# Performance work log

Measured on AMD Instinct MI355X. Metric: run time of the kernel, lower is better.

Reference implementation:

```python
import jax, jax.numpy as jnp
import numpy as np

N_NODES = 50000
N_EDGES = 800000
IN_SIZE = 128
NUM_HEADS = 8
HEAD_DIM = IN_SIZE // NUM_HEADS  # qk/val head dim = 16


def setup_inputs() -> dict:
    key = jax.random.key(0)
    ks = jax.random.split(key, 16)
    d = IN_SIZE
    lim = 1.0 / np.sqrt(d)
    inp = {
        "in_feats": jax.random.normal(ks[0], (N_NODES, d), jnp.float32),
        "struc_feats": jax.random.normal(ks[1], (N_NODES, d), jnp.float32),
        "edge_weights": jax.random.uniform(ks[2], (N_EDGES,), jnp.float32),
        "ln_scale": jnp.ones((d,), jnp.float32),
        "ln_bias": jnp.zeros((d,), jnp.float32),
        "Ws": jax.random.uniform(ks[3], (d, d), jnp.float32, -lim, lim),
        "bs": jnp.zeros((d,), jnp.float32),
        "Wq": jax.random.uniform(ks[4], (d, d), jnp.float32, -lim, lim),
        "bq": jnp.zeros((d,), jnp.float32),
        "Wk": jax.random.uniform(ks[5], (d, d), jnp.float32, -lim, lim),
        "bk": jnp.zeros((d,), jnp.float32),
        "Wv": jax.random.uniform(ks[6], (d, d), jnp.float32, -lim, lim),
        "bv": jnp.zeros((d,), jnp.float32),
        "Wo": jax.random.uniform(ks[7], (d, d), jnp.float32, -lim, lim),
        "edge_ids": jax.random.randint(ks[8], (2, N_EDGES), 0, N_NODES, jnp.int64)
        if jax.config.jax_enable_x64 else jax.random.randint(ks[8], (2, N_EDGES), 0, N_NODES, jnp.int32),
    }
    return inp


def _layer_norm(x, scale, bias, eps=1e-5):
    mu = jnp.mean(x, axis=-1, keepdims=True)
    var = jnp.var(x, axis=-1, keepdims=True)
    return (x - mu) * jax.lax.rsqrt(var + eps) * scale + bias


def reference(in_feats, struc_feats, edge_weights, ln_scale, ln_bias,
              Ws, bs, Wq, bq, Wk, bk, Wv, bv, Wo, edge_ids):
    N = in_feats.shape[0]
    H, hd = NUM_HEADS, HEAD_DIM

    delta = _layer_norm(in_feats, ln_scale, ln_bias)           # pre-norm
    delta = jax.nn.gelu(delta, approximate=False)               # pre-activation (exact GELU, torch default)
    delta_struc = delta + struc_feats @ Ws.T + bs               # struc_proj add

    qry = (delta_struc @ Wq.T + bq) / np.sqrt(hd)                # [N, qk]
    keyf = delta_struc @ Wk.T + bk                               # [N, qk]
    val = delta @ Wv.T + bv                                      # [N, val]

    src, dst = edge_ids[0], edge_ids[1]                          # out[src] += A[src,dst] * val[dst]
    qe = qry[src].reshape(-1, H, hd)                             # [E, H, hd]
    ke = keyf[dst].reshape(-1, H, hd)                            # [E, H, hd]
    attn = jax.nn.sigmoid(jnp.sum(qe * ke, axis=-1))             # [E, H]
    attn = edge_weights[:, None] * attn

    msgs = attn[:, :, None] * val[dst].reshape(-1, H, hd)        # [E, H, hd]
    agg = jax.ops.segment_sum(msgs.reshape(-1, H * hd), src, num_segments=N)  # [N, val]

    out = agg @ Wo.T                                             # out_proj (no bias)
    return in_feats + out                                        # skip connection
```

## Files before the change

kernel.cpp:

```cpp
#include <hip/hip_runtime.h>
#include <math.h>

#define NF 128

typedef __attribute__((ext_vector_type(8))) short short8;
typedef __attribute__((ext_vector_type(4))) float floatx4;

__device__ __forceinline__ unsigned short f2bf(float f) {
    union { float x; unsigned int i; } c; c.x = f;
    unsigned int r = c.i + 0x7fffu + ((c.i >> 16) & 1u);
    return (unsigned short)(r >> 16);
}
__device__ __forceinline__ float bf2f(unsigned short u) {
    union { unsigned int i; float x; } c; c.i = ((unsigned int)u) << 16;
    return c.x;
}
__device__ __forceinline__ void unpack8(uint4 u, float* f) {
    union { unsigned int i; float x; } c;
    c.i = u.x << 16;          f[0] = c.x;
    c.i = u.x & 0xffff0000u;  f[1] = c.x;
    c.i = u.y << 16;          f[2] = c.x;
    c.i = u.y & 0xffff0000u;  f[3] = c.x;
    c.i = u.z << 16;          f[4] = c.x;
    c.i = u.z & 0xffff0000u;  f[5] = c.x;
    c.i = u.w << 16;          f[6] = c.x;
    c.i = u.w & 0xffff0000u;  f[7] = c.x;
}
__device__ __forceinline__ ushort4 pack4(float a, float b, float c, float d) {
    ushort4 h; h.x = f2bf(a); h.y = f2bf(b); h.z = f2bf(c); h.w = f2bf(d);
    return h;
}

__global__ __launch_bounds__(256) void wconv5_kernel(
    const float* __restrict__ a, const float* __restrict__ b,
    const float* __restrict__ c, const float* __restrict__ d,
    const float* __restrict__ e, unsigned short* __restrict__ o)
{
    int i = blockIdx.x * 256 + threadIdx.x;
    int w = i >> 14, j = i & 16383;
    const float* p = (w == 0) ? a : (w == 1) ? b : (w == 2) ? c : (w == 3) ? d : e;
    o[i] = f2bf(p[j]);
}

__global__ __launch_bounds__(256) void node_a_kernel(
    const float* __restrict__ in_feats, const float* __restrict__ struc,
    const float* __restrict__ gamma, const float* __restrict__ beta,
    const unsigned short* __restrict__ Wsb, const float* __restrict__ bs,
    unsigned short* __restrict__ deltab, unsigned short* __restrict__ dstrb,
    int M, int nt)
{
    __shared__ unsigned short Wl[128][136];
    __shared__ unsigned short Xs2[64][136];

    int tid = threadIdx.x;
    int lane = tid & 63, w = tid >> 6, lg = lane & 15, quad = lane >> 4;
    int lrow = tid >> 2, t4 = tid & 3;

    {
        const uint4* g = (const uint4*)Wsb;
        #pragma unroll
        for (int p = 0; p < 8; ++p) {
            int idx = tid + p * 256;
            *(uint4*)&Wl[idx >> 4][(idx & 15) * 8] = g[idx];
        }
    }
    float bsr[8];
    #pragma unroll
    for (int t = 0; t < 8; ++t) bsr[t] = bs[t * 16 + lg];
    __syncthreads();

    for (int tile = blockIdx.x; tile < nt; tile += gridDim.x) {
        int m0 = tile * 64;
        int gm = m0 + lrow;
        bool vr = gm < M;
        size_t rbase = (size_t)(vr ? gm : 0) * NF;

        uint dreg[16];
        {
            const float4* ip = (const float4*)(in_feats + rbase) + t4 * 8;
            float4 xf[8];
            #pragma unroll
            for (int p = 0; p < 8; ++p) xf[p] = ip[p];
            float s = 0.f, sq = 0.f;
            #pragma unroll
            for (int p = 0; p < 8; ++p) {
                s  += xf[p].x + xf[p].y + xf[p].z + xf[p].w;
                sq += xf[p].x * xf[p].x + xf[p].y * xf[p].y
                    + xf[p].z * xf[p].z + xf[p].w * xf[p].w;
            }
            s  += __shfl_xor(s, 1, 64);  s  += __shfl_xor(s, 2, 64);
            sq += __shfl_xor(sq, 1, 64); sq += __shfl_xor(sq, 2, 64);
            float mu = s * (1.0f / 128.0f);
            float var = sq * (1.0f / 128.0f) - mu * mu;
            float rstd = rsqrtf(var + 1e-5f);
            const float4* gp = (const float4*)gamma + t4 * 8;
            const float4* bp = (const float4*)beta + t4 * 8;
            #pragma unroll
            for (int p = 0; p < 8; ++p) {
                float4 g4 = gp[p], b4 = bp[p];
                float o0 = (xf[p].x - mu) * rstd * g4.x + b4.x;
                float o1 = (xf[p].y - mu) * rstd * g4.y + b4.y;
                float o2 = (xf[p].z - mu) * rstd * g4.z + b4.z;
                float o3 = (xf[p].w - mu) * rstd * g4.w + b4.w;
                o0 = 0.5f * o0 * (1.0f + erff(o0 * 0.70710678118654752f));
                o1 = 0.5f * o1 * (1.0f + erff(o1 * 0.70710678118654752f));
                o2 = 0.5f * o2 * (1.0f + erff(o2 * 0.70710678118654752f));
                o3 = 0.5f * o3 * (1.0f + erff(o3 * 0.70710678118654752f));
                ushort4 h = pack4(o0, o1, o2, o3);
                dreg[p * 2]     = (uint)h.x | ((uint)h.y << 16);
                dreg[p * 2 + 1] = (uint)h.z | ((uint)h.w << 16);
            }
            if (vr) {
                uint4* od = (uint4*)(deltab + (size_t)gm * NF + t4 * 32);
                #pragma unroll
                for (int q = 0; q < 4; ++q)
                    od[q] = make_uint4(dreg[q*4], dreg[q*4+1], dreg[q*4+2], dreg[q*4+3]);
            }
            const float4* sp = (const float4*)(struc + rbase) + t4 * 8;
            #pragma unroll
            for (int p = 0; p < 8; ++p) {
                float4 f = sp[p];
                *(ushort4*)&Xs2[lrow][t4 * 32 + p * 4] = pack4(f.x, f.y, f.z, f.w);
            }
        }

        floatx4 acc[8];
        #pragma unroll
        for (int t = 0; t < 8; ++t) acc[t] = (floatx4){0.f, 0.f, 0.f, 0.f};
        #pragma unroll
        for (int ks = 0; ks < 4; ++ks) {
            short8 a = *(const short8*)&Xs2[w * 16 + lg][ks * 32 + quad * 8];
            #pragma unroll
            for (int t = 0; t < 8; ++t) {
                short8 b = *(const short8*)&Wl[t * 16 + lg][ks * 32 + quad * 8];
                acc[t] = __builtin_amdgcn_mfma_f32_16x16x32_bf16(a, b, acc[t], 0, 0, 0);
            }
        }

        #pragma unroll
        for (int q = 0; q < 4; ++q)
            *(uint4*)&Xs2[lrow][t4 * 32 + q * 8] =
                make_uint4(dreg[q*4], dreg[q*4+1], dreg[q*4+2], dreg[q*4+3]);

        #pragma unroll
        for (int t = 0; t < 8; ++t) {
            int col = t * 16 + lg;
            #pragma unroll
            for (int r = 0; r < 4; ++r) {
                int rl = w * 16 + quad * 4 + r;
                Xs2[rl][col] = f2bf(acc[t][r] + bsr[t] + bf2f(Xs2[rl][col]));
            }
        }
        #pragma unroll
        for (int p = 0; p < 4; ++p) {
            int idx = lane + p * 64;
            int row = w * 16 + (idx >> 4), c16 = idx & 15;
            int gmo = m0 + row;
            if (gmo < M)
                *(uint4*)(dstrb + (size_t)gmo * NF + c16 * 8) = *(const uint4*)&Xs2[row][c16 * 8];
        }
    }
}

__global__ __launch_bounds__(256) void node_qkv_kernel(
    const unsigned short* __restrict__ deltab, const unsigned short* __restrict__ dstrb,
    const unsigned short* __restrict__ Wall, const float* __restrict__ bq,
    const float* __restrict__ bk, const float* __restrict__ bv,
    unsigned short* __restrict__ qb, unsigned short* __restrict__ kvb,
    int M, int nt)
{
    __shared__ unsigned short Wl[128][136];
    __shared__ unsigned short Cst[64][136];

    int tid = threadIdx.x;
    int y = blockIdx.y;
    int lane = tid & 63, w = tid >> 6, lg = lane & 15, quad = lane >> 4;

    const unsigned short* Xg = (y == 2) ? deltab : dstrb;
    const unsigned short* Wg = Wall + (y + 1) * 16384;
    const float* bias = (y == 0) ? bq : (y == 1) ? bk : bv;
    float scale = (y == 0) ? 0.25f : 1.0f;
    unsigned short* outg = (y == 0) ? qb : (y == 1) ? kvb : (kvb + NF);
    int ostride = (y == 0) ? NF : 2 * NF;

    {
        const uint4* g = (const uint4*)Wg;
        #pragma unroll
        for (int p = 0; p < 8; ++p) {
            int idx = tid + p * 256;
            *(uint4*)&Wl[idx >> 4][(idx & 15) * 8] = g[idx];
        }
    }
    float br[8];
    #pragma unroll
    for (int t = 0; t < 8; ++t) br[t] = bias[t * 16 + lg] * scale;
    __syncthreads();

    for (int tile = blockIdx.x; tile < nt; tile += gridDim.x) {
        int m0 = tile * 64;
        int am = m0 + w * 16 + lg;
        const unsigned short* arow = Xg + (size_t)(am < M ? am : 0) * NF + quad * 8;

        floatx4 acc[8];
        #pragma unroll
        for (int t = 0; t < 8; ++t) acc[t] = (floatx4){0.f, 0.f, 0.f, 0.f};
        short8 af[4];
        #pragma unroll
        for (int ks = 0; ks < 4; ++ks) af[ks] = *(const short8*)(arow + ks * 32);
        #pragma unroll
        for (int ks = 0; ks < 4; ++ks) {
            #pragma unroll
            for (int t = 0; t < 8; ++t) {
                short8 b = *(const short8*)&Wl[t * 16 + lg][ks * 32 + quad * 8];
                acc[t] = __builtin_amdgcn_mfma_f32_16x16x32_bf16(af[ks], b, acc[t], 0, 0, 0);
            }
        }
        #pragma unroll
        for (int t = 0; t < 8; ++t) {
            int col = t * 16 + lg;
            #pragma unroll
            for (int r = 0; r < 4; ++r)
                Cst[w * 16 + quad * 4 + r][col] = f2bf(acc[t][r] * scale + br[t]);
        }
        #pragma unroll
        for (int p = 0; p < 4; ++p) {
            int idx = lane + p * 64;
            int row = w * 16 + (idx >> 4), c16 = idx & 15;
            int gm = m0 + row;
            if (gm < M)
                *(uint4*)(outg + (size_t)gm * ostride + c16 * 8) = *(const uint4*)&Cst[row][c16 * 8];
        }
    }
}

__global__ __launch_bounds__(256) void gemm_out_kernel(
    const unsigned short* __restrict__ Xb, const unsigned short* __restrict__ Wb,
    const float* __restrict__ addf, float* __restrict__ Y, int M, int nt)
{
    __shared__ unsigned short Wl[128][136];
    int tid = threadIdx.x;
    int lane = tid & 63, w = tid >> 6, lg = lane & 15, quad = lane >> 4;

    {
        const uint4* g = (const uint4*)Wb;
        #pragma unroll
        for (int p = 0; p < 8; ++p) {
            int idx = tid + p * 256;
            *(uint4*)&Wl[idx >> 4][(idx & 15) * 8] = g[idx];
        }
    }
    __syncthreads();

    for (int tile = blockIdx.x; tile < nt; tile += gridDim.x) {
        int m0 = tile * 64;
        int am = m0 + w * 16 + lg;
        const unsigned short* arow = Xb + (size_t)(am < M ? am : 0) * NF + quad * 8;

        floatx4 acc[8];
        #pragma unroll
        for (int t = 0; t < 8; ++t) acc[t] = (floatx4){0.f, 0.f, 0.f, 0.f};
        short8 af[4];
        #pragma unroll
        for (int ks = 0; ks < 4; ++ks) af[ks] = *(const short8*)(arow + ks * 32);
        #pragma unroll
        for (int ks = 0; ks < 4; ++ks) {
            #pragma unroll
            for (int t = 0; t < 8; ++t) {
                short8 b = *(const short8*)&Wl[t * 16 + lg][ks * 32 + quad * 8];
                acc[t] = __builtin_amdgcn_mfma_f32_16x16x32_bf16(af[ks], b, acc[t], 0, 0, 0);
            }
        }
        #pragma unroll
        for (int t = 0; t < 8; ++t) {
            int col = t * 16 + lg;
            #pragma unroll
            for (int r = 0; r < 4; ++r) {
                int gm = m0 + w * 16 + quad * 4 + r;
                if (gm >= M) continue;
                size_t off = (size_t)gm * NF + col;
                Y[off] = acc[t][r] + addf[off];
            }
        }
    }
}

__global__ void hist_kernel(const int* __restrict__ eid, int* __restrict__ cnt, int E)
{
    int i = blockIdx.x * blockDim.x + threadIdx.x;
    if (i < E) atomicAdd(&cnt[eid[i]], 1);
}

__global__ __launch_bounds__(256) void scan1_kernel(
    const int* __restrict__ cnt, int* __restrict__ bsum, int n)
{
    int base = blockIdx.x * 1024;
    int s = 0;
    #pragma unroll
    for (int p = 0; p < 4; ++p) {
        int i = base + (int)threadIdx.x + p * 256;
        if (i < n) s += cnt[i];
    }
    #pragma unroll
    for (int m = 1; m <= 32; m <<= 1) s += __shfl_xor(s, m, 64);
    __shared__ int ws_[4];
    int wid = threadIdx.x >> 6;
    if ((threadIdx.x & 63) == 0) ws_[wid] = s;
    __syncthreads();
    if (threadIdx.x == 0) bsum[blockIdx.x] = ws_[0] + ws_[1] + ws_[2] + ws_[3];
}

__global__ __launch_bounds__(256) void scan3_kernel(
    const int* __restrict__ cnt, const int* __restrict__ bsum,
    int* __restrict__ row_start, int* __restrict__ cursor, int n, int nb)
{
    __shared__ int base_off;
    int tid = threadIdx.x, lane = tid & 63, wid = tid >> 6;
    if (tid == 0) {
        int a = 0;
        for (int j = 0; j < (int)blockIdx.x; ++j) a += bsum[j];
        base_off = a;
        if ((int)blockIdx.x == nb - 1) {
            int tot = a;
            for (int j = blockIdx.x; j < nb; ++j) tot += bsum[j];
            row_start[n] = tot;
        }
    }
    int base = blockIdx.x * 1024;
    int v[4]; int s = 0;
    #pragma unroll
    for (int p = 0; p < 4; ++p) {
        int i = base + tid * 4 + p;
        v[p] = (i < n) ? cnt[i] : 0;
        s += v[p];
    }
    int ss = s;
    #pragma unroll
    for (int off = 1; off < 64; off <<= 1) {
        int t = __shfl_up(ss, off, 64);
        if (lane >= off) ss += t;
    }
    __shared__ int wsum[4];
    if (lane == 63) wsum[wid] = ss;
    __syncthreads();
    int woff = 0;
    for (int j = 0; j < wid; ++j) woff += wsum[j];
    int a = base_off + woff + (ss - s);
    #pragma unroll
    for (int p = 0; p < 4; ++p) {
        int i = base + tid * 4 + p;
        if (i < n) { row_start[i] = a; cursor[i] = a; a += v[p]; }
    }
}

__global__ void scatter_kernel(const int* __restrict__ eid, const float* __restrict__ ew,
                               int* __restrict__ cursor, int2* __restrict__ edata, int E)
{
    int i = blockIdx.x * blockDim.x + threadIdx.x;
    if (i < E) {
        int src = eid[i];
        int dst = eid[E + i];
        int pos = atomicAdd(&cursor[src], 1);
        edata[pos] = make_int2(dst, __float_as_int(ew[i]));
    }
}

__global__ __launch_bounds__(256) void aggregate_kernel(
    const unsigned short* __restrict__ Q, const unsigned short* __restrict__ kvb,
    const int* __restrict__ row_start, const int2* __restrict__ edata,
    unsigned short* __restrict__ agg, int N)
{
    int node = blockIdx.x * 4 + (threadIdx.x >> 6);
    if (node >= N) return;
    int lane = threadIdx.x & 63;
    int sg = lane >> 4, lg = lane & 15;
    int rs = row_start[node], re = row_start[node + 1];

    float qv[8];
    unpack8(*(const uint4*)(Q + (size_t)node * NF + lg * 8), qv);
    float acc[8];
    #pragma unroll
    for (int j = 0; j < 8; ++j) acc[j] = 0.f;

    int e1 = rs + sg, e2 = rs + sg + 4;
    int2 ed1 = (e1 < re) ? edata[e1] : make_int2(0, 0);
    int2 ed2 = (e2 < re) ? edata[e2] : make_int2(0, 0);

    for (int e0 = rs; e0 < re; e0 += 8) {
        int2 c1 = ed1, c2 = ed2;
        int en1 = e0 + 8 + sg, en2 = en1 + 4;
        ed1 = (en1 < re) ? edata[en1] : make_int2(0, 0);
        ed2 = (en2 < re) ? edata[en2] : make_int2(0, 0);

        const uint4* p1 = (const uint4*)kvb + (size_t)c1.x * 32 + lg;
        const uint4* p2 = (const uint4*)kvb + (size_t)c2.x * 32 + lg;
        uint4 k1u = p1[0], v1u = p1[16];
        uint4 k2u = p2[0], v2u = p2[16];

        float kv1[8], kv2[8];
        unpack8(k1u, kv1);
        unpack8(k2u, kv2);
        float s1 = qv[0] * kv1[0], s2 = qv[0] * kv2[0];
        #pragma unroll
        for (int j = 1; j < 8; ++j) {
            s1 = fmaf(qv[j], kv1[j], s1);
            s2 = fmaf(qv[j], kv2[j], s2);
        }
        s1 += __shfl_xor(s1, 1, 64);
        s2 += __shfl_xor(s2, 1, 64);
        float a1 = __int_as_float(c1.y) / (1.f + __expf(-s1));
        float a2 = __int_as_float(c2.y) / (1.f + __expf(-s2));

        float vv1[8], vv2[8];
        unpack8(v1u, vv1);
        unpack8(v2u, vv2);
        #pragma unroll
        for (int j = 0; j < 8; ++j) {
            acc[j] = fmaf(a1, vv1[j], acc[j]);
            acc[j] = fmaf(a2, vv2[j], acc[j]);
        }
    }
    #pragma unroll
    for (int j = 0; j < 8; ++j) {
        acc[j] += __shfl_xor(acc[j], 16, 64);
        acc[j] += __shfl_xor(acc[j], 32, 64);
    }
    if (sg == 0) {
        unsigned short* o = agg + (size_t)node * NF + lg * 8;
        *(ushort4*)o       = pack4(acc[0], acc[1], acc[2], acc[3]);
        *(ushort4*)(o + 4) = pack4(acc[4], acc[5], acc[6], acc[7]);
    }
}

extern "C" void kernel_launch(void* const* d_in, const int* in_sizes, int n_in,
                              void* d_out, int out_size, void* d_ws, size_t ws_size,
                              hipStream_t stream)
{
    const float* in_feats = (const float*)d_in[0];
    const float* struc    = (const float*)d_in[1];
    const float* eweights = (const float*)d_in[2];
    const float* ln_scale = (const float*)d_in[3];
    const float* ln_bias  = (const float*)d_in[4];
    const float* Ws       = (const float*)d_in[5];
    const float* bs       = (const float*)d_in[6];
    const float* Wq       = (const float*)d_in[7];
    const float* bq       = (const float*)d_in[8];
    const float* Wk       = (const float*)d_in[9];
    const float* bk       = (const float*)d_in[10];
    const float* Wv       = (const float*)d_in[11];
    const float* bv       = (const float*)d_in[12];
    const float* Wo       = (const float*)d_in[13];
    const int*   edge_ids = (const int*)d_in[14];
    float* out = (float*)d_out;

    int N = in_sizes[0] / NF;
    int E = in_sizes[2];

    size_t F = (size_t)N * NF;
    unsigned short* deltab = (unsigned short*)d_ws;
    unsigned short* dstrb  = deltab + F;
    unsigned short* qb     = dstrb + F;
    unsigned short* kvb    = qb + F;
    unsigned short* aggb   = kvb + 2 * F;
    unsigned short* Wall   = aggb + F;
    int2*  edata     = (int2*)(Wall + 5 * 16384);
    int*   cnt       = (int*)(edata + E);
    int*   row_start = cnt + N;
    int*   cursor    = row_start + N + 1;
    int*   bsum      = cursor + N;

    int nt  = (N + 63) / 64;
    int geb = (E + 255) / 256;
    int nb  = (N + 1023) / 1024;

    wconv5_kernel<<<(5 * 16384) / 256, 256, 0, stream>>>(Ws, Wq, Wk, Wv, Wo, Wall);

    hipMemsetAsync(cnt, 0, (size_t)N * sizeof(int), stream);
    hist_kernel<<<geb, 256, 0, stream>>>(edge_ids, cnt, E);
    scan1_kernel<<<nb, 256, 0, stream>>>(cnt, bsum, N);
    scan3_kernel<<<nb, 256, 0, stream>>>(cnt, bsum, row_start, cursor, N, nb);
    scatter_kernel<<<geb, 256, 0, stream>>>(edge_ids, eweights, cursor, edata, E);

    node_a_kernel<<<392, 256, 0, stream>>>(in_feats, struc, ln_scale, ln_bias,
                                           Wall, bs, deltab, dstrb, N, nt);
    node_qkv_kernel<<<dim3(261, 3), 256, 0, stream>>>(deltab, dstrb, Wall,
                                                      bq, bk, bv, qb, kvb, N, nt);

    aggregate_kernel<<<(N + 3) / 4, 256, 0, stream>>>(qb, kvb, row_start, edata, aggb, N);

    gemm_out_kernel<<<392, 256, 0, stream>>>(aggb, Wall + 4 * 16384, in_feats, out, N, nt);
}
```

Measured before the change: 327.7 us.

## Fuse pre-norm/struct projection with Q/K/V projections into one node kernel

Merges the layer-norm/GELU/struct-projection kernel and the three-way Q/K/V projection kernel into a single per-tile kernel. The delta and delta_struc tiles stay in shared memory instead of being written to and re-read from global bf16 buffers. Weight fragments are now read straight from global memory, relying on L1/L2, instead of being staged in LDS. Grid sizes for this kernel and the output GEMM become one block per tile. This removes the intermediate global traffic and a launch, but adds repeated global/cache reads of all four weight matrices per tile and serialises four GEMMs inside each block.

```diff
diff --git a/kernel.cpp b/kernel.cpp
--- a/kernel.cpp
+++ b/kernel.cpp
@@ -42,32 +42,36 @@
     o[i] = f2bf(p[j]);
 }
 
-__global__ __launch_bounds__(256) void node_a_kernel(
+__global__ __launch_bounds__(256) void node_fused_kernel(
     const float* __restrict__ in_feats, const float* __restrict__ struc,
     const float* __restrict__ gamma, const float* __restrict__ beta,
-    const unsigned short* __restrict__ Wsb, const float* __restrict__ bs,
-    unsigned short* __restrict__ deltab, unsigned short* __restrict__ dstrb,
+    const unsigned short* __restrict__ Wall,
+    const float* __restrict__ bs, const float* __restrict__ bq,
+    const float* __restrict__ bk, const float* __restrict__ bv,
+    unsigned short* __restrict__ qb, unsigned short* __restrict__ kvb,
     int M, int nt)
 {
-    __shared__ unsigned short Wl[128][136];
-    __shared__ unsigned short Xs2[64][136];
+    __shared__ unsigned short Xs[64][136];
+    __shared__ unsigned short XD[64][136];
+    __shared__ unsigned short Cst[64][136];
 
     int tid = threadIdx.x;
     int lane = tid & 63, w = tid >> 6, lg = lane & 15, quad = lane >> 4;
     int lrow = tid >> 2, t4 = tid & 3;
 
-    {
-        const uint4* g = (const uint4*)Wsb;
-        #pragma unroll
-        for (int p = 0; p < 8; ++p) {
-            int idx = tid + p * 256;
-            *(uint4*)&Wl[idx >> 4][(idx & 15) * 8] = g[idx];
-        }
-    }
-    float bsr[8];
-    #pragma unroll
-    for (int t = 0; t < 8; ++t) bsr[t] = bs[t * 16 + lg];
-    __syncthreads();
+    const unsigned short* Wsg = Wall;
+    const unsigned short* Wqg = Wall + 16384;
+    const unsigned short* Wkg = Wall + 2 * 16384;
+    const unsigned short* Wvg = Wall + 3 * 16384;
+
+    float bsr[8], bqr[8], bkr[8], bvr[8];
+    #pragma unroll
+    for (int t = 0; t < 8; ++t) {
+        bsr[t] = bs[t * 16 + lg];
+        bqr[t] = bq[t * 16 + lg] * 0.25f;
+        bkr[t] = bk[t * 16 + lg];
+        bvr[t] = bv[t * 16 + lg];
+    }
 
     for (int tile = blockIdx.x; tile < nt; tile += gridDim.x) {
         int m0 = tile * 64;
@@ -110,46 +114,62 @@
                 dreg[p * 2]     = (uint)h.x | ((uint)h.y << 16);
                 dreg[p * 2 + 1] = (uint)h.z | ((uint)h.w << 16);
             }
-            if (vr) {
-                uint4* od = (uint4*)(deltab + (size_t)gm * NF + t4 * 32);
-                #pragma unroll
-                for (int q = 0; q < 4; ++q)
-                    od[q] = make_uint4(dreg[q*4], dreg[q*4+1], dreg[q*4+2], dreg[q*4+3]);
-            }
+            #pragma unroll
+            for (int q = 0; q < 4; ++q)
+                *(uint4*)&XD[lrow][t4 * 32 + q * 8] =
+                    make_uint4(dreg[q*4], dreg[q*4+1], dreg[q*4+2], dreg[q*4+3]);
             const float4* sp = (const float4*)(struc + rbase) + t4 * 8;
             #pragma unroll
             for (int p = 0; p < 8; ++p) {
                 float4 f = sp[p];
-                *(ushort4*)&Xs2[lrow][t4 * 32 + p * 4] = pack4(f.x, f.y, f.z, f.w);
+                *(ushort4*)&Xs[lrow][t4 * 32 + p * 4] = pack4(f.x, f.y, f.z, f.w);
             }
         }
 
         floatx4 acc[8];
+
         #pragma unroll
         for (int t = 0; t < 8; ++t) acc[t] = (floatx4){0.f, 0.f, 0.f, 0.f};
         #pragma unroll
         for (int ks = 0; ks < 4; ++ks) {
-            short8 a = *(const short8*)&Xs2[w * 16 + lg][ks * 32 + quad * 8];
+            short8 a = *(const short8*)&Xs[w * 16 + lg][ks * 32 + quad * 8];
             #pragma unroll
             for (int t = 0; t < 8; ++t) {
-                short8 b = *(const short8*)&Wl[t * 16 + lg][ks * 32 + quad * 8];
+                short8 b = *(const short8*)(Wsg + ((t * 16 + lg) << 7) + ks * 32 + quad * 8);
                 acc[t] = __builtin_amdgcn_mfma_f32_16x16x32_bf16(a, b, acc[t], 0, 0, 0);
             }
         }
-
         #pragma unroll
         for (int q = 0; q < 4; ++q)
-            *(uint4*)&Xs2[lrow][t4 * 32 + q * 8] =
+            *(uint4*)&Xs[lrow][t4 * 32 + q * 8] =
                 make_uint4(dreg[q*4], dreg[q*4+1], dreg[q*4+2], dreg[q*4+3]);
-
         #pragma unroll
         for (int t = 0; t < 8; ++t) {
             int col = t * 16 + lg;
             #pragma unroll
             for (int r = 0; r < 4; ++r) {
                 int rl = w * 16 + quad * 4 + r;
-                Xs2[rl][col] = f2bf(acc[t][r] + bsr[t] + bf2f(Xs2[rl][col]));
-            }
+                Xs[rl][col] = f2bf(acc[t][r] + bsr[t] + bf2f(Xs[rl][col]));
+            }
+        }
+
+        #pragma unroll
+        for (int t = 0; t < 8; ++t) acc[t] = (floatx4){0.f, 0.f, 0.f, 0.f};
+        #pragma unroll
+        for (int ks = 0; ks < 4; ++ks) {
+            short8 a = *(const short8*)&XD[w * 16 + lg][ks * 32 + quad * 8];
+            #pragma unroll
+            for (int t = 0; t < 8; ++t) {
+                short8 b = *(const short8*)(Wvg + ((t * 16 + lg) << 7) + ks * 32 + quad * 8);
+                acc[t] = __builtin_amdgcn_mfma_f32_16x16x32_bf16(a, b, acc[t], 0, 0, 0);
+            }
+        }
+        #pragma unroll
+        for (int t = 0; t < 8; ++t) {
+            int col = t * 16 + lg;
+            #pragma unroll
+            for (int r = 0; r < 4; ++r)
+                Cst[w * 16 + quad * 4 + r][col] = f2bf(acc[t][r] + bvr[t]);
         }
         #pragma unroll
         for (int p = 0; p < 4; ++p) {
@@ -157,62 +177,18 @@
             int row = w * 16 + (idx >> 4), c16 = idx & 15;
             int gmo = m0 + row;
             if (gmo < M)
-                *(uint4*)(dstrb + (size_t)gmo * NF + c16 * 8) = *(const uint4*)&Xs2[row][c16 * 8];
-        }
-    }
-}
-
-__global__ __launch_bounds__(256) void node_qkv_kernel(
-    const unsigned short* __restrict__ deltab, const unsigned short* __restrict__ dstrb,
-    const unsigned short* __restrict__ Wall, const float* __restrict__ bq,
-    const float* __restrict__ bk, const float* __restrict__ bv,
-    unsigned short* __restrict__ qb, unsigned short* __restrict__ kvb,
-    int M, int nt)
-{
-    __shared__ unsigned short Wl[128][136];
-    __shared__ unsigned short Cst[64][136];
-
-    int tid = threadIdx.x;
-    int y = blockIdx.y;
-    int lane = tid & 63, w = tid >> 6, lg = lane & 15, quad = lane >> 4;
-
-    const unsigned short* Xg = (y == 2) ? deltab : dstrb;
-    const unsigned short* Wg = Wall + (y + 1) * 16384;
-    const float* bias = (y == 0) ? bq : (y == 1) ? bk : bv;
-    float scale = (y == 0) ? 0.25f : 1.0f;
-    unsigned short* outg = (y == 0) ? qb : (y == 1) ? kvb : (kvb + NF);
-    int ostride = (y == 0) ? NF : 2 * NF;
-
-    {
-        const uint4* g = (const uint4*)Wg;
-        #pragma unroll
-        for (int p = 0; p < 8; ++p) {
-            int idx = tid + p * 256;
-            *(uint4*)&Wl[idx >> 4][(idx & 15) * 8] = g[idx];
-        }
-    }
-    float br[8];
-    #pragma unroll
-    for (int t = 0; t < 8; ++t) br[t] = bias[t * 16 + lg] * scale;
-    __syncthreads();
-
-    for (int tile = blockIdx.x; tile < nt; tile += gridDim.x) {
-        int m0 = tile * 64;
-        int am = m0 + w * 16 + lg;
-        const unsigned short* arow = Xg + (size_t)(am < M ? am : 0) * NF + quad * 8;
-
-        floatx4 acc[8];
+                *(uint4*)(kvb + (size_t)gmo * 2 * NF + NF + c16 * 8) = *(const uint4*)&Cst[row][c16 * 8];
+        }
+
         #pragma unroll
         for (int t = 0; t < 8; ++t) acc[t] = (floatx4){0.f, 0.f, 0.f, 0.f};
-        short8 af[4];
-        #pragma unroll
-        for (int ks = 0; ks < 4; ++ks) af[ks] = *(const short8*)(arow + ks * 32);
         #pragma unroll
         for (int ks = 0; ks < 4; ++ks) {
+            short8 a = *(const short8*)&Xs[w * 16 + lg][ks * 32 + quad * 8];
             #pragma unroll
             for (int t = 0; t < 8; ++t) {
-                short8 b = *(const short8*)&Wl[t * 16 + lg][ks * 32 + quad * 8];
-                acc[t] = __builtin_amdgcn_mfma_f32_16x16x32_bf16(af[ks], b, acc[t], 0, 0, 0);
+                short8 b = *(const short8*)(Wqg + ((t * 16 + lg) << 7) + ks * 32 + quad * 8);
+                acc[t] = __builtin_amdgcn_mfma_f32_16x16x32_bf16(a, b, acc[t], 0, 0, 0);
             }
         }
         #pragma unroll
@@ -220,15 +196,42 @@
             int col = t * 16 + lg;
             #pragma unroll
             for (int r = 0; r < 4; ++r)
-                Cst[w * 16 + quad * 4 + r][col] = f2bf(acc[t][r] * scale + br[t]);
+                Cst[w * 16 + quad * 4 + r][col] = f2bf(acc[t][r] * 0.25f + bqr[t]);
         }
         #pragma unroll
         for (int p = 0; p < 4; ++p) {
             int idx = lane + p * 64;
             int row = w * 16 + (idx >> 4), c16 = idx & 15;
-            int gm = m0 + row;
-            if (gm < M)
-                *(uint4*)(outg + (size_t)gm * ostride + c16 * 8) = *(const uint4*)&Cst[row][c16 * 8];
+            int gmo = m0 + row;
+            if (gmo < M)
+                *(uint4*)(qb + (size_t)gmo * NF + c16 * 8) = *(const uint4*)&Cst[row][c16 * 8];
+        }
+
+        #pragma unroll
+        for (int t = 0; t < 8; ++t) acc[t] = (floatx4){0.f, 0.f, 0.f, 0.f};
+        #pragma unroll
+        for (int ks = 0; ks < 4; ++ks) {
+            short8 a = *(const short8*)&Xs[w * 16 + lg][ks * 32 + quad * 8];
+            #pragma unroll
+            for (int t = 0; t < 8; ++t) {
+                short8 b = *(const short8*)(Wkg + ((t * 16 + lg) << 7) + ks * 32 + quad * 8);
+                acc[t] = __builtin_amdgcn_mfma_f32_16x16x32_bf16(a, b, acc[t], 0, 0, 0);
+            }
+        }
+        #pragma unroll
+        for (int t = 0; t < 8; ++t) {
+            int col = t * 16 + lg;
+            #pragma unroll
+            for (int r = 0; r < 4; ++r)
+                Cst[w * 16 + quad * 4 + r][col] = f2bf(acc[t][r] + bkr[t]);
+        }
+        #pragma unroll
+        for (int p = 0; p < 4; ++p) {
+            int idx = lane + p * 64;
+            int row = w * 16 + (idx >> 4), c16 = idx & 15;
+            int gmo = m0 + row;
+            if (gmo < M)
+                *(uint4*)(kvb + (size_t)gmo * 2 * NF + c16 * 8) = *(const uint4*)&Cst[row][c16 * 8];
         }
     }
 }
@@ -456,9 +459,7 @@
     int E = in_sizes[2];
 
     size_t F = (size_t)N * NF;
-    unsigned short* deltab = (unsigned short*)d_ws;
-    unsigned short* dstrb  = deltab + F;
-    unsigned short* qb     = dstrb + F;
+    unsigned short* qb     = (unsigned short*)d_ws;
     unsigned short* kvb    = qb + F;
     unsigned short* aggb   = kvb + 2 * F;
     unsigned short* Wall   = aggb + F;
@@ -480,12 +481,10 @@
     scan3_kernel<<<nb, 256, 0, stream>>>(cnt, bsum, row_start, cursor, N, nb);
     scatter_kernel<<<geb, 256, 0, stream>>>(edge_ids, eweights, cursor, edata, E);
 
-    node_a_kernel<<<392, 256, 0, stream>>>(in_feats, struc, ln_scale, ln_bias,
-                                           Wall, bs, deltab, dstrb, N, nt);
-    node_qkv_kernel<<<dim3(261, 3), 256, 0, stream>>>(deltab, dstrb, Wall,
-                                                      bq, bk, bv, qb, kvb, N, nt);
+    node_fused_kernel<<<nt, 256, 0, stream>>>(in_feats, struc, ln_scale, ln_bias,
+                                              Wall, bs, bq, bk, bv, qb, kvb, N, nt);
 
     aggregate_kernel<<<(N + 3) / 4, 256, 0, stream>>>(qb, kvb, row_start, edata, aggb, N);
 
-    gemm_out_kernel<<<392, 256, 0, stream>>>(aggb, Wall + 4 * 16384, in_feats, out, N, nt);
-}
+    gemm_out_kernel<<<nt, 256, 0, stream>>>(aggb, Wall + 4 * 16384, in_feats, out, N, nt);
+}
```

New measurement: 489.8 us. +49.5%, slower.

## Split node pipeline into LN, struc/V GEMM, and Q/K GEMM kernels

Applied to the files above, without the earlier changes.

The fused LayerNorm+struc-projection kernel is split into a standalone LayerNorm/GELU kernel and a GEMM kernel that computes the struc projection and the V projection as two grid slices. A Q/K GEMM kernel follows, so each kernel has more independent blocks and less serial work per block. The count-array memset is folded into the weight-conversion kernel, and the output GEMM now launches one block per tile. The cost is an extra launch and re-reading deltab from global memory in the epilogue instead of reusing registers.

```diff
diff --git a/kernel.cpp b/kernel.cpp
--- a/kernel.cpp
+++ b/kernel.cpp
@@ -31,97 +31,129 @@
     return h;
 }
 
-__global__ __launch_bounds__(256) void wconv5_kernel(
+__global__ __launch_bounds__(256) void wconv5z_kernel(
     const float* __restrict__ a, const float* __restrict__ b,
     const float* __restrict__ c, const float* __restrict__ d,
-    const float* __restrict__ e, unsigned short* __restrict__ o)
-{
-    int i = blockIdx.x * 256 + threadIdx.x;
-    int w = i >> 14, j = i & 16383;
-    const float* p = (w == 0) ? a : (w == 1) ? b : (w == 2) ? c : (w == 3) ? d : e;
-    o[i] = f2bf(p[j]);
-}
-
-__global__ __launch_bounds__(256) void node_a_kernel(
-    const float* __restrict__ in_feats, const float* __restrict__ struc,
-    const float* __restrict__ gamma, const float* __restrict__ beta,
-    const unsigned short* __restrict__ Wsb, const float* __restrict__ bs,
-    unsigned short* __restrict__ deltab, unsigned short* __restrict__ dstrb,
-    int M, int nt)
+    const float* __restrict__ e, unsigned short* __restrict__ o,
+    int* __restrict__ cnt, int N)
+{
+    int blk = blockIdx.x;
+    if (blk < 320) {
+        int i = blk * 256 + threadIdx.x;
+        int w = i >> 14, j = i & 16383;
+        const float* p = (w == 0) ? a : (w == 1) ? b : (w == 2) ? c : (w == 3) ? d : e;
+        o[i] = f2bf(p[j]);
+    } else {
+        int i = (blk - 320) * 256 + threadIdx.x;
+        if (i < N) cnt[i] = 0;
+    }
+}
+
+__global__ __launch_bounds__(256) void ln_kernel(
+    const float* __restrict__ in_feats, const float* __restrict__ gamma,
+    const float* __restrict__ beta, unsigned short* __restrict__ deltab, int M)
+{
+    int gi = blockIdx.x * 256 + threadIdx.x;
+    int row = gi >> 2, t4 = gi & 3;
+    if (row >= M) return;
+    size_t rbase = (size_t)row * NF;
+
+    const float4* ip = (const float4*)(in_feats + rbase) + t4 * 8;
+    float4 xf[8];
+    #pragma unroll
+    for (int p = 0; p < 8; ++p) xf[p] = ip[p];
+    float s = 0.f, sq = 0.f;
+    #pragma unroll
+    for (int p = 0; p < 8; ++p) {
+        s  += xf[p].x + xf[p].y + xf[p].z + xf[p].w;
+        sq += xf[p].x * xf[p].x + xf[p].y * xf[p].y
+            + xf[p].z * xf[p].z + xf[p].w * xf[p].w;
+    }
+    s  += __shfl_xor(s, 1, 64);  s  += __shfl_xor(s, 2, 64);
+    sq += __shfl_xor(sq, 1, 64); sq += __shfl_xor(sq, 2, 64);
+    float mu = s * (1.0f / 128.0f);
+    float var = sq * (1.0f / 128.0f) - mu * mu;
+    float rstd = rsqrtf(var + 1e-5f);
+
+    const float4* gp = (const float4*)gamma + t4 * 8;
+    const float4* bp = (const float4*)beta + t4 * 8;
+    uint dreg[16];
+    #pragma unroll
+    for (int p = 0; p < 8; ++p) {
+        float4 g4 = gp[p], b4 = bp[p];
+        float o0 = (xf[p].x - mu) * rstd * g4.x + b4.x;
+        float o1 = (xf[p].y - mu) * rstd * g4.y + b4.y;
+        float o2 = (xf[p].z - mu) * rstd * g4.z + b4.z;
+        float o3 = (xf[p].w - mu) * rstd * g4.w + b4.w;
+        o0 = 0.5f * o0 * (1.0f + erff(o0 * 0.70710678118654752f));
+        o1 = 0.5f * o1 * (1.0f + erff(o1 * 0.70710678118654752f));
+        o2 = 0.5f * o2 * (1.0f + erff(o2 * 0.70710678118654752f));
+        o3 = 0.5f * o3 * (1.0f + erff(o3 * 0.70710678118654752f));
+        ushort4 h = pack4(o0, o1, o2, o3);
+        dreg[p * 2]     = (uint)h.x | ((uint)h.y << 16);
+        dreg[p * 2 + 1] = (uint)h.z | ((uint)h.w << 16);
+    }
+    uint4* od = (uint4*)(deltab + rbase + t4 * 32);
+    #pragma unroll
+    for (int q = 0; q < 4; ++q)
+        od[q] = make_uint4(dreg[q*4], dreg[q*4+1], dreg[q*4+2], dreg[q*4+3]);
+}
+
+__global__ __launch_bounds__(256) void gemm_dv_kernel(
+    const float* __restrict__ struc, const unsigned short* __restrict__ deltab,
+    const unsigned short* __restrict__ Wall, const float* __restrict__ bs,
+    const float* __restrict__ bv, unsigned short* __restrict__ dstrb,
+    unsigned short* __restrict__ kvb, int M, int nt)
 {
     __shared__ unsigned short Wl[128][136];
-    __shared__ unsigned short Xs2[64][136];
+    __shared__ unsigned short Cst[64][136];
 
     int tid = threadIdx.x;
+    int y = blockIdx.y;
     int lane = tid & 63, w = tid >> 6, lg = lane & 15, quad = lane >> 4;
-    int lrow = tid >> 2, t4 = tid & 3;
+
+    const unsigned short* Wg = Wall + ((y == 0) ? 0 : 3 * 16384);
+    const float* bias = (y == 0) ? bs : bv;
+    unsigned short* outg = (y == 0) ? dstrb : (kvb + NF);
+    int ostride = (y == 0) ? NF : 2 * NF;
 
     {
-        const uint4* g = (const uint4*)Wsb;
+        const uint4* g = (const uint4*)Wg;
         #pragma unroll
         for (int p = 0; p < 8; ++p) {
             int idx = tid + p * 256;
             *(uint4*)&Wl[idx >> 4][(idx & 15) * 8] = g[idx];
         }
     }
-    float bsr[8];
-    #pragma unroll
-    for (int t = 0; t < 8; ++t) bsr[t] = bs[t * 16 + lg];
+    float br[8];
+    #pragma unroll
+    for (int t = 0; t < 8; ++t) br[t] = bias[t * 16 + lg];
     __syncthreads();
 
     for (int tile = blockIdx.x; tile < nt; tile += gridDim.x) {
         int m0 = tile * 64;
-        int gm = m0 + lrow;
-        bool vr = gm < M;
-        size_t rbase = (size_t)(vr ? gm : 0) * NF;
-
-        uint dreg[16];
-        {
-            const float4* ip = (const float4*)(in_feats + rbase) + t4 * 8;
-            float4 xf[8];
-            #pragma unroll
-            for (int p = 0; p < 8; ++p) xf[p] = ip[p];
-            float s = 0.f, sq = 0.f;
-            #pragma unroll
-            for (int p = 0; p < 8; ++p) {
-                s  += xf[p].x + xf[p].y + xf[p].z + xf[p].w;
-                sq += xf[p].x * xf[p].x + xf[p].y * xf[p].y
-                    + xf[p].z * xf[p].z + xf[p].w * xf[p].w;
-            }
-            s  += __shfl_xor(s, 1, 64);  s  += __shfl_xor(s, 2, 64);
-            sq += __shfl_xor(sq, 1, 64); sq += __shfl_xor(sq, 2, 64);
-            float mu = s * (1.0f / 128.0f);
-            float var = sq * (1.0f / 128.0f) - mu * mu;
-            float rstd = rsqrtf(var + 1e-5f);
-            const float4* gp = (const float4*)gamma + t4 * 8;
-            const float4* bp = (const float4*)beta + t4 * 8;
-            #pragma unroll
-            for (int p = 0; p < 8; ++p) {
-                float4 g4 = gp[p], b4 = bp[p];
-                float o0 = (xf[p].x - mu) * rstd * g4.x + b4.x;
-                float o1 = (xf[p].y - mu) * rstd * g4.y + b4.y;
-                float o2 = (xf[p].z - mu) * rstd * g4.z + b4.z;
-                float o3 = (xf[p].w - mu) * rstd * g4.w + b4.w;
-                o0 = 0.5f * o0 * (1.0f + erff(o0 * 0.70710678118654752f));
-                o1 = 0.5f * o1 * (1.0f + erff(o1 * 0.70710678118654752f));
-                o2 = 0.5f * o2 * (1.0f + erff(o2 * 0.70710678118654752f));
-                o3 = 0.5f * o3 * (1.0f + erff(o3 * 0.70710678118654752f));
-                ushort4 h = pack4(o0, o1, o2, o3);
-                dreg[p * 2]     = (uint)h.x | ((uint)h.y << 16);
-                dreg[p * 2 + 1] = (uint)h.z | ((uint)h.w << 16);
-            }
-            if (vr) {
-                uint4* od = (uint4*)(deltab + (size_t)gm * NF + t4 * 32);
-                #pragma unroll
-                for (int q = 0; q < 4; ++q)
-                    od[q] = make_uint4(dreg[q*4], dreg[q*4+1], dreg[q*4+2], dreg[q*4+3]);
-            }
-            const float4* sp = (const float4*)(struc + rbase) + t4 * 8;
-            #pragma unroll
-            for (int p = 0; p < 8; ++p) {
-                float4 f = sp[p];
-                *(ushort4*)&Xs2[lrow][t4 * 32 + p * 4] = pack4(f.x, f.y, f.z, f.w);
-            }
+        int am = m0 + w * 16 + lg;
+        size_t rb = (size_t)(am < M ? am : 0) * NF;
+
+        short8 af[4];
+        if (y == 0) {
+            const float4* sp = (const float4*)(struc + rb);
+            #pragma unroll
+            for (int ks = 0; ks < 4; ++ks) {
+                float4 f0 = sp[ks * 8 + quad * 2];
+                float4 f1 = sp[ks * 8 + quad * 2 + 1];
+                ushort4 h0 = pack4(f0.x, f0.y, f0.z, f0.w);
+                ushort4 h1 = pack4(f1.x, f1.y, f1.z, f1.w);
+                uint4 pk = make_uint4((uint)h0.x | ((uint)h0.y << 16),
+                                      (uint)h0.z | ((uint)h0.w << 16),
+                                      (uint)h1.x | ((uint)h1.y << 16),
+                                      (uint)h1.z | ((uint)h1.w << 16));
+                af[ks] = *(short8*)&pk;
+            }
+        } else {
+            const unsigned short* arow = deltab + rb + quad * 8;
+            #pragma unroll
+            for (int ks = 0; ks < 4; ++ks) af[ks] = *(const short8*)(arow + ks * 32);
         }
 
         floatx4 acc[8];
@@ -129,43 +161,47 @@
         for (int t = 0; t < 8; ++t) acc[t] = (floatx4){0.f, 0.f, 0.f, 0.f};
         #pragma unroll
         for (int ks = 0; ks < 4; ++ks) {
-            short8 a = *(const short8*)&Xs2[w * 16 + lg][ks * 32 + quad * 8];
             #pragma unroll
             for (int t = 0; t < 8; ++t) {
                 short8 b = *(const short8*)&Wl[t * 16 + lg][ks * 32 + quad * 8];
-                acc[t] = __builtin_amdgcn_mfma_f32_16x16x32_bf16(a, b, acc[t], 0, 0, 0);
-            }
-        }
-
-        #pragma unroll
-        for (int q = 0; q < 4; ++q)
-            *(uint4*)&Xs2[lrow][t4 * 32 + q * 8] =
-                make_uint4(dreg[q*4], dreg[q*4+1], dreg[q*4+2], dreg[q*4+3]);
-
-        #pragma unroll
-        for (int t = 0; t < 8; ++t) {
-            int col = t * 16 + lg;
-            #pragma unroll
-            for (int r = 0; r < 4; ++r) {
-                int rl = w * 16 + quad * 4 + r;
-                Xs2[rl][col] = f2bf(acc[t][r] + bsr[t] + bf2f(Xs2[rl][col]));
+                acc[t] = __builtin_amdgcn_mfma_f32_16x16x32_bf16(af[ks], b, acc[t], 0, 0, 0);
+            }
+        }
+
+        if (y == 0) {
+            #pragma unroll
+            for (int t = 0; t < 8; ++t) {
+                int col = t * 16 + lg;
+                #pragma unroll
+                for (int r = 0; r < 4; ++r) {
+                    int gm = m0 + w * 16 + quad * 4 + r;
+                    float dadd = bf2f(deltab[(size_t)(gm < M ? gm : 0) * NF + col]);
+                    Cst[w * 16 + quad * 4 + r][col] = f2bf(acc[t][r] + br[t] + dadd);
+                }
+            }
+        } else {
+            #pragma unroll
+            for (int t = 0; t < 8; ++t) {
+                int col = t * 16 + lg;
+                #pragma unroll
+                for (int r = 0; r < 4; ++r)
+                    Cst[w * 16 + quad * 4 + r][col] = f2bf(acc[t][r] + br[t]);
             }
         }
         #pragma unroll
         for (int p = 0; p < 4; ++p) {
             int idx = lane + p * 64;
             int row = w * 16 + (idx >> 4), c16 = idx & 15;
-            int gmo = m0 + row;
-            if (gmo < M)
-                *(uint4*)(dstrb + (size_t)gmo * NF + c16 * 8) = *(const uint4*)&Xs2[row][c16 * 8];
-        }
-    }
-}
-
-__global__ __launch_bounds__(256) void node_qkv_kernel(
-    const unsigned short* __restrict__ deltab, const unsigned short* __restrict__ dstrb,
-    const unsigned short* __restrict__ Wall, const float* __restrict__ bq,
-    const float* __restrict__ bk, const float* __restrict__ bv,
+            int gm = m0 + row;
+            if (gm < M)
+                *(uint4*)(outg + (size_t)gm * ostride + c16 * 8) = *(const uint4*)&Cst[row][c16 * 8];
+        }
+    }
+}
+
+__global__ __launch_bounds__(256) void gemm_qk_kernel(
+    const unsigned short* __restrict__ dstrb, const unsigned short* __restrict__ Wall,
+    const float* __restrict__ bq, const float* __restrict__ bk,
     unsigned short* __restrict__ qb, unsigned short* __restrict__ kvb,
     int M, int nt)
 {
@@ -176,11 +212,10 @@
     int y = blockIdx.y;
     int lane = tid & 63, w = tid >> 6, lg = lane & 15, quad = lane >> 4;
 
-    const unsigned short* Xg = (y == 2) ? deltab : dstrb;
     const unsigned short* Wg = Wall + (y + 1) * 16384;
-    const float* bias = (y == 0) ? bq : (y == 1) ? bk : bv;
+    const float* bias = (y == 0) ? bq : bk;
     float scale = (y == 0) ? 0.25f : 1.0f;
-    unsigned short* outg = (y == 0) ? qb : (y == 1) ? kvb : (kvb + NF);
+    unsigned short* outg = (y == 0) ? qb : kvb;
     int ostride = (y == 0) ? NF : 2 * NF;
 
     {
@@ -199,7 +234,7 @@
     for (int tile = blockIdx.x; tile < nt; tile += gridDim.x) {
         int m0 = tile * 64;
         int am = m0 + w * 16 + lg;
-        const unsigned short* arow = Xg + (size_t)(am < M ? am : 0) * NF + quad * 8;
+        const unsigned short* arow = dstrb + (size_t)(am < M ? am : 0) * NF + quad * 8;
 
         floatx4 acc[8];
         #pragma unroll
@@ -471,21 +506,23 @@
     int nt  = (N + 63) / 64;
     int geb = (E + 255) / 256;
     int nb  = (N + 1023) / 1024;
-
-    wconv5_kernel<<<(5 * 16384) / 256, 256, 0, stream>>>(Ws, Wq, Wk, Wv, Wo, Wall);
-
-    hipMemsetAsync(cnt, 0, (size_t)N * sizeof(int), stream);
+    int zb  = (N + 255) / 256;
+    int lnb = (N * 4 + 255) / 256;
+
+    wconv5z_kernel<<<320 + zb, 256, 0, stream>>>(Ws, Wq, Wk, Wv, Wo, Wall, cnt, N);
+
     hist_kernel<<<geb, 256, 0, stream>>>(edge_ids, cnt, E);
     scan1_kernel<<<nb, 256, 0, stream>>>(cnt, bsum, N);
     scan3_kernel<<<nb, 256, 0, stream>>>(cnt, bsum, row_start, cursor, N, nb);
     scatter_kernel<<<geb, 256, 0, stream>>>(edge_ids, eweights, cursor, edata, E);
 
-    node_a_kernel<<<392, 256, 0, stream>>>(in_feats, struc, ln_scale, ln_bias,
-                                           Wall, bs, deltab, dstrb, N, nt);
-    node_qkv_kernel<<<dim3(261, 3), 256, 0, stream>>>(deltab, dstrb, Wall,
-                                                      bq, bk, bv, qb, kvb, N, nt);
+    ln_kernel<<<lnb, 256, 0, stream>>>(in_feats, ln_scale, ln_bias, deltab, N);
+    gemm_dv_kernel<<<dim3(261, 2), 256, 0, stream>>>(struc, deltab, Wall,
+                                                     bs, bv, dstrb, kvb, N, nt);
+    gemm_qk_kernel<<<dim3(261, 2), 256, 0, stream>>>(dstrb, Wall, bq, bk,
+                                                     qb, kvb, N, nt);
 
     aggregate_kernel<<<(N + 3) / 4, 256, 0, stream>>>(qb, kvb, row_start, edata, aggb, N);
 
-    gemm_out_kernel<<<392, 256, 0, stream>>>(aggb, Wall + 4 * 16384, in_feats, out, N, nt);
-}
+    gemm_out_kernel<<<nt, 256, 0, stream>>>(aggb, Wall + 4 * 16384, in_feats, out, N, nt);
+}
```

Measured after the change: 329.0 us. Within noise of the previous version (+0.4%).
